# Kernel tuning notes

Measured on AMD Instinct MI355X. Metric: run time of the kernel, lower is better.

## Reference

```python
import jax, jax.numpy as jnp
import numpy as np

B, Y, X, C = 32, 32, 32, 256
N, K = 8, 4            # query heads, kv groups
M = N // K             # query heads per group
DQ, DV = 32, 32        # qk / v head widths (invariant rep)
HQ = DQ // 2           # rotation pairs


def setup_inputs() -> dict:
    key = jax.random.key(0)
    ks = jax.random.split(key, 8)
    s = 1.0 / np.sqrt(C)
    return {
        'x':    jax.random.normal(ks[0], (B, Y, X, C), jnp.float32),
        'xpos': jax.random.uniform(ks[1], (X, 2), jnp.float32),
        'ypos': jax.random.uniform(ks[2], (Y, 2), jnp.float32),
        'Wq':   jax.random.normal(ks[3], (C, 2, 2, 2, M, K, HQ, 2), jnp.float32) * s,
        'Wk':   jax.random.normal(ks[4], (C, 2, 2, 2, K, HQ, 2), jnp.float32) * s,
        'Wv':   jax.random.normal(ks[5], (C, 2, 2, 2, K, DV), jnp.float32) * s,
        'bv':   jnp.zeros((2, 2, 2, K, DV), jnp.float32),
        'Wo':   jax.random.normal(ks[6], (2, 2, 2, M, K, DV, C), jnp.float32) / np.sqrt(8 * N * DV),
        'rope_freq': jax.random.normal(ks[7], (M, K, HQ, 2), jnp.float32),
    }


def _rope_scaling():
    # pi / stack([linspace(1,30,HQ), linspace(0.1,1,HQ)]).T -> [HQ, 2]
    return jnp.asarray(np.pi / np.stack([np.linspace(1.0, 30.0, HQ),
                                         np.linspace(0.1, 1.0, HQ)], axis=-1).astype(np.float32))


def _rot(freq, pos):
    # freq [M,K,HQ,2], pos [L,2] -> rotation matrices [L, 2(dir), M, K, HQ, 2, 2]
    phi = jnp.einsum('mkhp,lp->lmkh', freq, pos)
    c, s = jnp.cos(phi), jnp.sin(phi)
    # idx = [[[0,2],[1,0]],[[0,1],[2,0]]] over (cos, sin, -sin): fwd and inverse rotation
    r_fwd = jnp.stack([jnp.stack([c, -s], -1), jnp.stack([s, c], -1)], -2)
    r_bwd = jnp.stack([jnp.stack([c, s], -1), jnp.stack([-s, c], -1)], -2)
    return jnp.stack([r_fwd, r_bwd], axis=1)


def reference(x, xpos, ypos, Wq, Wk, Wv, bv, Wo, rope_freq):
    freq = rope_freq * _rope_scaling()                       # [M,K,HQ,2]
    # projections: a=axis(2), d=direction(2), v=chirality(2)
    q = jnp.einsum('byxc,cadvmkhp->byxadvmkhp', x, Wq)
    k = jnp.einsum('byxc,cadvkhp->byxadvkhp', x, Wk)
    vv = jnp.einsum('byxc,cadvkh->byxadvkh', x, Wv) + bv

    outs = []
    for axis, pos in ((0, ypos), (1, xpos)):
        rot = _rot(freq, pos)                                # [L,d,M,K,HQ,2,2]
        qa = q[:, :, :, axis]                                # [B,Y,X,d,v,M,K,HQ,2]
        ka = k[:, :, :, axis]                                # [B,Y,X,d,v,K,HQ,2]
        va = vv[:, :, :, axis]                               # [B,Y,X,d,v,K,DV]
        if axis == 0:  # attend along Y
            Qr = jnp.einsum('byxdvmkhp,ydmkhpq->byxdvmkhq', qa, rot)
            Kr = jnp.einsum('byxdvkhp,ydmkhpq->byxdvmkhq', ka, rot)
            sc = jax.nn.sigmoid(jnp.einsum('btxdvmkhq,bsxdvmkhq->btsxdvmk', Qr, Kr))
            o = jnp.einsum('btsxdvmk,bsxdvkh->btxdvmkh', sc, va)
        else:          # attend along X
            Qr = jnp.einsum('byxdvmkhp,xdmkhpq->byxdvmkhq', qa, rot)
            Kr = jnp.einsum('byxdvkhp,xdmkhpq->byxdvmkhq', ka, rot)
            sc = jax.nn.sigmoid(jnp.einsum('bytdvmkhq,bysdvmkhq->bytsdvmk', Qr, Kr))
            o = jnp.einsum('bytsdvmk,bysdvkh->bytdvmkh', sc, va)
        outs.append(o)                                       # [B,Y,X,d,v,M,K,DV]
    V = jnp.stack(outs, axis=3)                              # [B,Y,X,a,d,v,M,K,DV]
    return jnp.einsum('byxadvmkh,advmkhc->byxc', V, Wo)
```

## Files before the change

### kernel.cpp

```cpp
#include <hip/hip_runtime.h>
#include <math.h>

namespace {

typedef __attribute__((ext_vector_type(8))) short short8;
typedef __attribute__((ext_vector_type(4))) float f32x4;

constexpr float kPI = 3.14159265358979323846f;

__device__ __forceinline__ unsigned short f2bf(float f) {
    unsigned int u = __float_as_uint(f);
    u += 0x7fffu + ((u >> 16) & 1u);
    return (unsigned short)(u >> 16);
}

__device__ __forceinline__ short8 pack8(const float* f) {
    short8 r;
    #pragma unroll
    for (int i = 0; i < 8; ++i) r[i] = (short)f2bf(f[i]);
    return r;
}

__device__ __forceinline__ f32x4 MFMA(short8 a, short8 b, f32x4 c) {
    return __builtin_amdgcn_mfma_f32_16x16x32_bf16(a, b, c, 0, 0, 0);
}

__global__ __launch_bounds__(256)
void prep_weights(const float* __restrict__ Wq, const float* __restrict__ Wk,
                  const float* __restrict__ Wv, const float* __restrict__ Wo,
                  short* __restrict__ wsQ, short* __restrict__ wsKV,
                  short* __restrict__ wsO)
{
    const int cid = blockIdx.x * 4 + (threadIdx.x >> 6);
    const int l = threadIdx.x & 63;
    const int lr = l & 15, lk = l >> 4;
    const int arr = cid >> 10, c2 = cid & 1023;
    const int adv = c2 >> 7, ks = (c2 >> 4) & 7, nt = c2 & 15;
    const int c0 = ks * 32 + lk * 8;
    float v[8];
    if (arr == 0) {
        const int j = nt * 16 + lr;
        #pragma unroll
        for (int i = 0; i < 8; ++i)
            v[i] = Wq[((size_t)(c0 + i) * 8 + adv) * 256 + j];
    } else if (arr == 1) {
        if (nt < 8) {
            const int j = nt * 16 + lr;
            #pragma unroll
            for (int i = 0; i < 8; ++i)
                v[i] = Wk[((size_t)(c0 + i) * 8 + adv) * 128 + j];
        } else {
            const int j = (nt - 8) * 16 + lr;
            #pragma unroll
            for (int i = 0; i < 8; ++i)
                v[i] = Wv[((size_t)(c0 + i) * 8 + adv) * 128 + j];
        }
    } else {
        const int cc = nt * 16 + lr;
        #pragma unroll
        for (int i = 0; i < 8; ++i)
            v[i] = Wo[((size_t)adv * 256 + (c0 + i)) * 256 + cc];
    }
    short* dst = (arr == 0 ? wsQ : arr == 1 ? wsKV : wsO) + (size_t)c2 * 512 + l * 8;
    *(short8*)dst = pack8(v);
}

template <int AXIS, bool ACCUM>
__global__ __launch_bounds__(512, 4)
void axial_attn_mfma(const float* __restrict__ x,
                     const float* __restrict__ xpos,
                     const float* __restrict__ ypos,
                     const float* __restrict__ bvp,
                     const float* __restrict__ rfreq,
                     const short* __restrict__ wsQ,
                     const short* __restrict__ wsKV,
                     const short* __restrict__ wsO,
                     float* __restrict__ out)
{
    __shared__ __align__(16) short xs[32 * 256];
    __shared__ __align__(16) short qbuf[32 * 256];
    __shared__ __align__(16) short kbuf[32 * 256];
    __shared__ __align__(16) short vbuf[4 * 32 * 32];
    __shared__ __align__(16) short obuf[32 * 256];
    __shared__ float2 posf[32];
    __shared__ float2 rfs[128];

    const int t = threadIdx.x;
    const int b = blockIdx.x >> 5;
    const int line = blockIdx.x & 31;
    const int w = t >> 6, l = t & 63;
    const int lr = l & 15, lk = l >> 4;
    const int p01 = l & 1;

    {
        const int row = t >> 4;
        const int c0 = (t & 15) * 16;
        const int gy = (AXIS == 0) ? row : line;
        const int gx = (AXIS == 0) ? line : row;
        const float* px = x + ((size_t)((b * 32 + gy) * 32 + gx)) * 256 + c0;
        float tmp[16];
        #pragma unroll
        for (int i = 0; i < 16; i += 4) {
            const float4 a = *(const float4*)(px + i);
            tmp[i] = a.x; tmp[i + 1] = a.y; tmp[i + 2] = a.z; tmp[i + 3] = a.w;
        }
        const int swz = (row & 7) << 3;
        *(short8*)&xs[row * 256 + (c0 ^ swz)] = pack8(tmp);
        *(short8*)&xs[row * 256 + ((c0 + 8) ^ swz)] = pack8(tmp + 8);
    }
    const float* posv = (AXIS == 0) ? ypos : xpos;
    if (t < 128) {
        const int h = t & 15;
        const float s0 = kPI / (1.0f + (29.0f / 15.0f) * (float)h);
        const float s1 = kPI / (0.1f + 0.06f * (float)h);
        rfs[t] = make_float2(rfreq[2 * t] * s0, rfreq[2 * t + 1] * s1);
    }
    if (t < 32) posf[t] = make_float2(posv[2 * t], posv[2 * t + 1]);
    __syncthreads();

    f32x4 oacc[2][2] = {};
    const short8* wsQv  = (const short8*)wsQ;
    const short8* wsKVv = (const short8*)wsKV;
    const short8* wsOv  = (const short8*)wsO;
    const int m_w = w >> 2, kk_w = w & 3;
    const int aswz = (lr & 7) << 3;

    for (int dvi = 0; dvi < 4; ++dvi) {
        const int adv = AXIS * 4 + dvi;
        const float sgn = (dvi < 2) ? 1.0f : -1.0f;

        {
            f32x4 acc[2][2] = {};
            #pragma unroll 2
            for (int ks = 0; ks < 8; ++ks) {
                const int e = (ks * 32 + lk * 8) ^ aswz;
                const short8 a0 = *(const short8*)&xs[lr * 256 + e];
                const short8 a1 = *(const short8*)&xs[(16 + lr) * 256 + e];
                const short8 b0 = wsQv[(size_t)((adv * 8 + ks) * 16 + w * 2 + 0) * 64 + l];
                const short8 b1 = wsQv[(size_t)((adv * 8 + ks) * 16 + w * 2 + 1) * 64 + l];
                acc[0][0] = MFMA(a0, b0, acc[0][0]);
                acc[1][0] = MFMA(a1, b0, acc[1][0]);
                acc[0][1] = MFMA(a0, b1, acc[0][1]);
                acc[1][1] = MFMA(a1, b1, acc[1][1]);
            }
            #pragma unroll 1
            for (int mt = 0; mt < 2; ++mt)
                #pragma unroll 1
                for (int nt = 0; nt < 2; ++nt) {
                    const int h = (nt * 16 + lr) >> 1;
                    const float2 rf = rfs[m_w * 64 + kk_w * 16 + h];
                    #pragma unroll
                    for (int r = 0; r < 4; ++r) {
                        const float own = acc[mt][nt][r];
                        const float oth = __shfl_xor(own, 1);
                        const int pos = mt * 16 + lk * 4 + r;
                        const float2 pp = posf[pos];
                        float sv, cv;
                        __sincosf(rf.x * pp.x + rf.y * pp.y, &sv, &cv);
                        const float rv = (p01 == 0) ? cv * own + sgn * sv * oth
                                                    : cv * own - sgn * sv * oth;
                        const int col = w * 32 + nt * 16 + lr;
                        qbuf[pos * 256 + (col ^ ((pos & 7) << 3))] = (short)f2bf(rv);
                    }
                }
        }

        {
            f32x4 acc[2][2] = {};
            #pragma unroll 2
            for (int ks = 0; ks < 8; ++ks) {
                const int e = (ks * 32 + lk * 8) ^ aswz;
                const short8 a0 = *(const short8*)&xs[lr * 256 + e];
                const short8 a1 = *(const short8*)&xs[(16 + lr) * 256 + e];
                const short8 b0 = wsKVv[(size_t)((adv * 8 + ks) * 16 + w * 2 + 0) * 64 + l];
                const short8 b1 = wsKVv[(size_t)((adv * 8 + ks) * 16 + w * 2 + 1) * 64 + l];
                acc[0][0] = MFMA(a0, b0, acc[0][0]);
                acc[1][0] = MFMA(a1, b0, acc[1][0]);
                acc[0][1] = MFMA(a0, b1, acc[0][1]);
                acc[1][1] = MFMA(a1, b1, acc[1][1]);
            }
            if (w < 4) {
                #pragma unroll 1
                for (int mt = 0; mt < 2; ++mt)
                    #pragma unroll 1
                    for (int nt = 0; nt < 2; ++nt) {
                        const int h = (nt * 16 + lr) >> 1;
                        const float2 rf0 = rfs[w * 16 + h];
                        const float2 rf1 = rfs[64 + w * 16 + h];
                        #pragma unroll
                        for (int r = 0; r < 4; ++r) {
                            const float own = acc[mt][nt][r];
                            const float oth = __shfl_xor(own, 1);
                            const int pos = mt * 16 + lk * 4 + r;
                            const float2 pp = posf[pos];
                            #pragma unroll
                            for (int m2 = 0; m2 < 2; ++m2) {
                                const float2 rf = (m2 == 0) ? rf0 : rf1;
                                float sv, cv;
                                __sincosf(rf.x * pp.x + rf.y * pp.y, &sv, &cv);
                                const float rv = (p01 == 0) ? cv * own + sgn * sv * oth
                                                            : cv * own - sgn * sv * oth;
                                const int col = (m2 * 4 + w) * 32 + nt * 16 + lr;
                                kbuf[pos * 256 + (col ^ ((pos & 7) << 3))] = (short)f2bf(rv);
                            }
                        }
                    }
            } else {
                const int kk = w - 4;
                #pragma unroll
                for (int nt = 0; nt < 2; ++nt) {
                    const int dv = nt * 16 + lr;
                    const float bvv = bvp[adv * 128 + kk * 32 + dv];
                    #pragma unroll
                    for (int mt = 0; mt < 2; ++mt)
                        #pragma unroll
                        for (int r = 0; r < 4; ++r) {
                            const int s = mt * 16 + lk * 4 + r;
                            vbuf[kk * 1024 + dv * 32 + (s ^ ((dv & 3) << 3))] =
                                (short)f2bf(acc[mt][nt][r] + bvv);
                        }
                }
            }
        }
        __syncthreads();

        {
            const int g = w;
            short8 ka[2], qa[2];
            #pragma unroll
            for (int st = 0; st < 2; ++st) {
                const int row = st * 16 + lr;
                ka[st] = *(const short8*)&kbuf[row * 256 + ((g * 32 + lk * 8) ^ ((row & 7) << 3))];
            }
            #pragma unroll
            for (int qt = 0; qt < 2; ++qt) {
                const int row = qt * 16 + lr;
                qa[qt] = *(const short8*)&qbuf[row * 256 + ((g * 32 + lk * 8) ^ ((row & 7) << 3))];
            }
            f32x4 d[2][2] = {};
            #pragma unroll
            for (int st = 0; st < 2; ++st)
                #pragma unroll
                for (int qt = 0; qt < 2; ++qt)
                    d[st][qt] = MFMA(ka[st], qa[qt], d[st][qt]);

            unsigned int pk[2][2][2];
            #pragma unroll
            for (int st = 0; st < 2; ++st)
                #pragma unroll
                for (int qt = 0; qt < 2; ++qt)
                    #pragma unroll
                    for (int h2 = 0; h2 < 2; ++h2) {
                        const float za = __builtin_amdgcn_rcpf(1.0f + __expf(-d[st][qt][2 * h2]));
                        const float zb = __builtin_amdgcn_rcpf(1.0f + __expf(-d[st][qt][2 * h2 + 1]));
                        pk[st][qt][h2] = (unsigned int)f2bf(za) |
                                         ((unsigned int)f2bf(zb) << 16);
                    }

            const int srcA = ((lk & 1) * 2) * 16 + lr;
            short8 pa[2];
            #pragma unroll
            for (int qt = 0; qt < 2; ++qt) {
                union { unsigned int u[4]; short8 s; } uu;
                #pragma unroll
                for (int jp = 0; jp < 4; ++jp) {
                    const int src = srcA + (jp >> 1) * 16;
                    const int v0 = __shfl((int)pk[0][qt][jp & 1], src, 64);
                    const int v1 = __shfl((int)pk[1][qt][jp & 1], src, 64);
                    uu.u[jp] = (lk < 2) ? (unsigned int)v0 : (unsigned int)v1;
                }
                pa[qt] = uu.s;
            }

            const int kkg = g & 3;
            short8 vb2[2];
            #pragma unroll
            for (int dvt = 0; dvt < 2; ++dvt) {
                const int dv = dvt * 16 + lr;
                vb2[dvt] = *(const short8*)&vbuf[kkg * 1024 + dv * 32 + ((lk * 8) ^ ((dv & 3) << 3))];
            }
            f32x4 o2[2][2] = {};
            #pragma unroll
            for (int qt = 0; qt < 2; ++qt)
                #pragma unroll
                for (int dvt = 0; dvt < 2; ++dvt)
                    o2[qt][dvt] = MFMA(pa[qt], vb2[dvt], o2[qt][dvt]);

            #pragma unroll
            for (int qt = 0; qt < 2; ++qt)
                #pragma unroll
                for (int dvt = 0; dvt < 2; ++dvt)
                    #pragma unroll
                    for (int r = 0; r < 4; ++r) {
                        const int q = qt * 16 + lk * 4 + r;
                        const int col = g * 32 + dvt * 16 + lr;
                        obuf[q * 256 + (col ^ ((q & 7) << 3))] = (short)f2bf(o2[qt][dvt][r]);
                    }
        }
        __syncthreads();

        {
            #pragma unroll 2
            for (int ks = 0; ks < 8; ++ks) {
                const int e = (ks * 32 + lk * 8) ^ aswz;
                const short8 a0 = *(const short8*)&obuf[lr * 256 + e];
                const short8 a1 = *(const short8*)&obuf[(16 + lr) * 256 + e];
                const short8 b0 = wsOv[(size_t)((adv * 8 + ks) * 16 + w * 2 + 0) * 64 + l];
                const short8 b1 = wsOv[(size_t)((adv * 8 + ks) * 16 + w * 2 + 1) * 64 + l];
                oacc[0][0] = MFMA(a0, b0, oacc[0][0]);
                oacc[1][0] = MFMA(a1, b0, oacc[1][0]);
                oacc[0][1] = MFMA(a0, b1, oacc[0][1]);
                oacc[1][1] = MFMA(a1, b1, oacc[1][1]);
            }
        }
    }

    #pragma unroll
    for (int mt = 0; mt < 2; ++mt)
        #pragma unroll
        for (int nt = 0; nt < 2; ++nt)
            #pragma unroll
            for (int r = 0; r < 4; ++r) {
                const int pos = mt * 16 + lk * 4 + r;
                const int c = w * 32 + nt * 16 + lr;
                const int gy = (AXIS == 0) ? pos : line;
                const int gx = (AXIS == 0) ? line : pos;
                float* po = out + ((size_t)((b * 32 + gy) * 32 + gx)) * 256 + c;
                if (ACCUM) *po += oacc[mt][nt][r];
                else       *po = oacc[mt][nt][r];
            }
}

}

extern "C" void kernel_launch(void* const* d_in, const int* in_sizes, int n_in,
                              void* d_out, int out_size, void* d_ws, size_t ws_size,
                              hipStream_t stream) {
    (void)in_sizes; (void)n_in; (void)out_size; (void)ws_size;
    const float* x     = (const float*)d_in[0];
    const float* xpos  = (const float*)d_in[1];
    const float* ypos  = (const float*)d_in[2];
    const float* Wq    = (const float*)d_in[3];
    const float* Wk    = (const float*)d_in[4];
    const float* Wv    = (const float*)d_in[5];
    const float* bv    = (const float*)d_in[6];
    const float* Wo    = (const float*)d_in[7];
    const float* rfreq = (const float*)d_in[8];
    float* out = (float*)d_out;

    short* wsQ  = (short*)d_ws;
    short* wsKV = wsQ + 1024 * 512;
    short* wsO  = wsKV + 1024 * 512;

    prep_weights<<<dim3(768), dim3(256), 0, stream>>>(Wq, Wk, Wv, Wo, wsQ, wsKV, wsO);
    axial_attn_mfma<0, false><<<dim3(1024), dim3(512), 0, stream>>>(
        x, xpos, ypos, bv, rfreq, wsQ, wsKV, wsO, out);
    axial_attn_mfma<1, true><<<dim3(1024), dim3(512), 0, stream>>>(
        x, xpos, ypos, bv, rfreq, wsQ, wsKV, wsO, out);
}
```

Baseline: 268.2 us.

## Merge both axial passes into one launch with atomic output accumulation

Replaces the two per-axis template launches with a single 2048-block launch where the low bit of the block index selects the axis. The output is zeroed with a memset and both axes accumulate into it with float atomicAdd. This removes a kernel boundary and the tail between the passes, and lets the two axes run concurrently. In exchange it adds a memset, atomic traffic on every output element, and runtime axis branching in place of compile-time specialisation. Summation order becomes nondeterministic.

```diff
diff --git a/kernel.cpp b/kernel.cpp
--- a/kernel.cpp
+++ b/kernel.cpp
@@ -65,7 +65,6 @@
     *(short8*)dst = pack8(v);
 }
 
-template <int AXIS, bool ACCUM>
 __global__ __launch_bounds__(512, 4)
 void axial_attn_mfma(const float* __restrict__ x,
                      const float* __restrict__ xpos,
@@ -86,8 +85,10 @@
     __shared__ float2 rfs[128];
 
     const int t = threadIdx.x;
-    const int b = blockIdx.x >> 5;
-    const int line = blockIdx.x & 31;
+    const int axis = blockIdx.x & 1;
+    const int bl = blockIdx.x >> 1;
+    const int b = bl >> 5;
+    const int line = bl & 31;
     const int w = t >> 6, l = t & 63;
     const int lr = l & 15, lk = l >> 4;
     const int p01 = l & 1;
@@ -95,8 +96,8 @@
     {
         const int row = t >> 4;
         const int c0 = (t & 15) * 16;
-        const int gy = (AXIS == 0) ? row : line;
-        const int gx = (AXIS == 0) ? line : row;
+        const int gy = (axis == 0) ? row : line;
+        const int gx = (axis == 0) ? line : row;
         const float* px = x + ((size_t)((b * 32 + gy) * 32 + gx)) * 256 + c0;
         float tmp[16];
         #pragma unroll
@@ -108,7 +109,7 @@
         *(short8*)&xs[row * 256 + (c0 ^ swz)] = pack8(tmp);
         *(short8*)&xs[row * 256 + ((c0 + 8) ^ swz)] = pack8(tmp + 8);
     }
-    const float* posv = (AXIS == 0) ? ypos : xpos;
+    const float* posv = (axis == 0) ? ypos : xpos;
     if (t < 128) {
         const int h = t & 15;
         const float s0 = kPI / (1.0f + (29.0f / 15.0f) * (float)h);
@@ -126,7 +127,7 @@
     const int aswz = (lr & 7) << 3;
 
     for (int dvi = 0; dvi < 4; ++dvi) {
-        const int adv = AXIS * 4 + dvi;
+        const int adv = axis * 4 + dvi;
         const float sgn = (dvi < 2) ? 1.0f : -1.0f;
 
         {
@@ -323,11 +324,10 @@
             for (int r = 0; r < 4; ++r) {
                 const int pos = mt * 16 + lk * 4 + r;
                 const int c = w * 32 + nt * 16 + lr;
-                const int gy = (AXIS == 0) ? pos : line;
-                const int gx = (AXIS == 0) ? line : pos;
-                float* po = out + ((size_t)((b * 32 + gy) * 32 + gx)) * 256 + c;
-                if (ACCUM) *po += oacc[mt][nt][r];
-                else       *po = oacc[mt][nt][r];
+                const int gy = (axis == 0) ? pos : line;
+                const int gx = (axis == 0) ? line : pos;
+                atomicAdd(out + ((size_t)((b * 32 + gy) * 32 + gx)) * 256 + c,
+                          oacc[mt][nt][r]);
             }
 }
 
@@ -336,7 +336,7 @@
 extern "C" void kernel_launch(void* const* d_in, const int* in_sizes, int n_in,
                               void* d_out, int out_size, void* d_ws, size_t ws_size,
                               hipStream_t stream) {
-    (void)in_sizes; (void)n_in; (void)out_size; (void)ws_size;
+    (void)in_sizes; (void)n_in; (void)ws_size;
     const float* x     = (const float*)d_in[0];
     const float* xpos  = (const float*)d_in[1];
     const float* ypos  = (const float*)d_in[2];
@@ -352,9 +352,8 @@
     short* wsKV = wsQ + 1024 * 512;
     short* wsO  = wsKV + 1024 * 512;
 
+    hipMemsetAsync(d_out, 0, (size_t)out_size * sizeof(float), stream);
     prep_weights<<<dim3(768), dim3(256), 0, stream>>>(Wq, Wk, Wv, Wo, wsQ, wsKV, wsO);
-    axial_attn_mfma<0, false><<<dim3(1024), dim3(512), 0, stream>>>(
+    axial_attn_mfma<<<dim3(2048), dim3(512), 0, stream>>>(
         x, xpos, ypos, bv, rfreq, wsQ, wsKV, wsO, out);
-    axial_attn_mfma<1, true><<<dim3(1024), dim3(512), 0, stream>>>(
-        x, xpos, ypos, bv, rfreq, wsQ, wsKV, wsO, out);
-}
+}
```

Measured after the change: 301.5 us. 1.12x slower.
